# Performance work log

Measured on AMD Instinct MI355X. Metric: run time of the kernel, lower is better.

Reference implementation:

```python
import jax, jax.numpy as jnp
import numpy as np

SIGMA = 4.0
KSIZE = 2 * int(4.0 * SIGMA + 0.5) + 1  # 33, anomalib AnomalyMapGenerator default


def _gauss_kernel():
    x = jnp.arange(KSIZE, dtype=jnp.float32) - (KSIZE - 1) / 2.0
    g = jnp.exp(-0.5 * (x / SIGMA) ** 2)
    return g / g.sum()


def _blur(img):
    # img: (B,1,H,W); separable Gaussian with reflect padding (kornia border_type='reflect')
    k = _gauss_kernel()
    p = (KSIZE - 1) // 2
    dn = ('NCHW', 'OIHW', 'NCHW')
    x = jnp.pad(img, ((0, 0), (0, 0), (p, p), (0, 0)), mode='reflect')
    x = jax.lax.conv_general_dilated(x, k.reshape(1, 1, KSIZE, 1), (1, 1), 'VALID', dimension_numbers=dn)
    x = jnp.pad(x, ((0, 0), (0, 0), (0, 0), (p, p)), mode='reflect')
    return jax.lax.conv_general_dilated(x, k.reshape(1, 1, 1, KSIZE), (1, 1), 'VALID', dimension_numbers=dn)


def _edist(x, y):
    # ||x-y||_2 via expanded quadratic, clamped at 0 (matches torch euclidean_dist)
    x2 = jnp.sum(x * x, axis=-1, keepdims=True)
    y2 = jnp.sum(y * y, axis=-1, keepdims=True)
    d2 = x2 - 2.0 * (x @ y.T) + y2.T
    return jnp.sqrt(jnp.clip(d2, 0.0))


def setup_inputs() -> dict:
    key = jax.random.key(0)
    k1, k2 = jax.random.split(key)
    return {
        'embedding': jax.random.normal(k1, (6272, 128), dtype=jnp.float32),
        'memory_bank': jax.random.normal(k2, (32768, 128), dtype=jnp.float32),
        'batch_size': 8,
        'width': 28,
        'height': 28,
        'out_size': 224,
        'num_neighbors': 9,
    }


def reference(embedding, memory_bank, batch_size, width, height, out_size, num_neighbors):
    N, D = embedding.shape
    M = memory_bank.shape[0]
    # --- nearest_neighbors(embedding, n_neighbors=1), euclidean metric ---
    dist = _edist(embedding, memory_bank)            # (N, M) dominant intermediate
    patch_scores = jnp.min(dist, axis=1)             # (N,)
    locations = jnp.argmin(dist, axis=1)             # (N,)
    P = N // batch_size
    patch_scores = patch_scores.reshape(batch_size, P)
    locations = locations.reshape(batch_size, P)
    # --- compute_anomaly_score (num_neighbors > 1 branch) ---
    b_idx = jnp.arange(batch_size)
    max_p = jnp.argmax(patch_scores, axis=1)                         # (B,)
    max_feat = embedding.reshape(batch_size, P, D)[b_idx, max_p]     # (B, D)
    score = patch_scores[b_idx, max_p]                               # (B,)
    nn_idx = locations[b_idx, max_p]                                 # (B,)
    nn_sample = memory_bank[nn_idx]                                  # (B, D)
    k = min(int(num_neighbors), M)
    d_nn = _edist(nn_sample, memory_bank)                            # (B, M)
    _, support = jax.lax.top_k(-d_nn, k)                             # (B, k) smallest distances
    mem_s = memory_bank[support]                                     # (B, k, D)
    qm = jnp.einsum('bd,bkd->bk', max_feat, mem_s)
    d2 = jnp.sum(max_feat * max_feat, -1, keepdims=True) - 2.0 * qm + jnp.sum(mem_s * mem_s, -1)
    dists = jnp.sqrt(jnp.clip(d2, 0.0))                              # (B, k)
    weights = (1.0 - jax.nn.softmax(dists, axis=1))[:, 0]
    pred_score = weights * score                                     # (B,)
    # --- anomaly map: bilinear upsample (align_corners=False) + Gaussian blur ---
    pm = patch_scores.reshape(batch_size, 1, width, height)
    amap = jax.image.resize(pm, (batch_size, 1, out_size, out_size), method='bilinear')
    anomaly_map = _blur(amap)
    return pred_score, anomaly_map
```

## Files before the change

### kernel.cpp

```cpp
#include <hip/hip_runtime.h>
#include <hip/hip_bf16.h>

#define N_EMB   6272
#define M_BANK  32768
#define D_DIM   128
#define KPA     128
#define KPB     128
#define BATCH   8
#define P_PATCH 784
#define GRID_WH 28
#define OUT_WH  224
#define KNN     9
#define KSIZE   33
#define KRAD    16

typedef unsigned long long ull;
typedef short bf16x8 __attribute__((ext_vector_type(8)));
typedef float f32x4  __attribute__((ext_vector_type(4)));

#define WS_MINPACK 0
#define WS_X2      50176
#define WS_Y2      75264
#define WS_BSCORE  231424
#define WS_BMAXP   231456
#define WS_BNN     231488
#define WS_DNN     231552
#define WS_APK     2885888
#define WS_BPK     7702784
#define WS_CAND    32868608

__device__ __forceinline__ ull umin64(ull a, ull b) { return a < b ? a : b; }
__device__ __forceinline__ ull umax64(ull a, ull b) { return a > b ? a : b; }

__device__ __forceinline__ void gload_lds16(const void* g, void* l) {
    __builtin_amdgcn_global_load_lds(
        (const __attribute__((address_space(1))) void*)g,
        (__attribute__((address_space(3))) void*)l, 16, 0, 0);
}

__device__ unsigned tpf_ctr = 0;

__global__ __launch_bounds__(256) void prep_kernel(
    const float* __restrict__ emb, const float* __restrict__ bank,
    unsigned short* __restrict__ Apk, unsigned short* __restrict__ Bpk,
    float* __restrict__ x2, float* __restrict__ y2, ull* __restrict__ minpack)
{
    const int tid = threadIdx.x;
    int gi = blockIdx.x * 256 + tid;
    if (gi < N_EMB) minpack[gi] = ~0ull;

    const int w    = blockIdx.x * 4 + (tid >> 6);
    const int lane = tid & 63;

    const float* src;
    unsigned short* dst;
    float* sq;
    if (w < N_EMB) {
        src = emb + (size_t)w * D_DIM;
        dst = Apk + (size_t)w * KPA;
        sq  = x2 + w;
    } else {
        int m = w - N_EMB;
        src = bank + (size_t)m * D_DIM;
        dst = Bpk + (size_t)m * KPB;
        sq  = y2 + m;
    }
    float2 v = *(const float2*)&src[2 * lane];
    __hip_bfloat16 h0 = __float2bfloat16(v.x);
    __hip_bfloat16 h1 = __float2bfloat16(v.y);
    unsigned hb0 = *(unsigned short*)&h0, hb1 = *(unsigned short*)&h1;
    *(unsigned*)&dst[2 * lane] = hb0 | (hb1 << 16);

    float s = fmaf(v.x, v.x, v.y * v.y);
    #pragma unroll
    for (int off = 32; off > 0; off >>= 1) s += __shfl_down(s, off, 64);
    if (lane == 0) *sq = s;
}

__global__ __launch_bounds__(256, 4) void mfma_min_kernel(
    const unsigned short* __restrict__ Apk, const unsigned short* __restrict__ Bpk,
    const float* __restrict__ y2, ull* __restrict__ minpack)
{
    __shared__ __align__(16) unsigned short smem[4 * 128 * 32];
    const int PAN = 128 * 32;

    const int tid  = threadIdx.x;
    const int lane = tid & 63;
    const int wave = tid >> 6;
    const int wr = wave >> 1, wc = wave & 1;
    const int n0 = blockIdx.y * 128;
    const int m0 = blockIdx.x * 128;

    const int srow = tid >> 2;
    const int sseg = tid & 3;
    const int ssw  = sseg ^ ((srow >> 1) & 3);

    const int qa = lane >> 4;
    const int ra = lane & 15;
    const int qsw = qa ^ ((ra >> 1) & 3);

    f32x4 acc[4][4];
    #pragma unroll
    for (int i = 0; i < 4; ++i)
        #pragma unroll
        for (int j = 0; j < 4; ++j)
            acc[i][j] = (f32x4){0.f, 0.f, 0.f, 0.f};

    const unsigned short* gA = Apk + (size_t)(n0 + srow) * KPA + ssw * 8;
    const unsigned short* gB = Bpk + (size_t)(m0 + srow) * KPB + ssw * 8;
    const int lof0 = srow * 32 + sseg * 8;
    const int lof1 = (srow + 64) * 32 + sseg * 8;

    gload_lds16(gA,            &smem[lof0]);
    gload_lds16(gA + 64 * KPA, &smem[lof1]);
    gload_lds16(gB,            &smem[2 * PAN + lof0]);
    gload_lds16(gB + 64 * KPB, &smem[2 * PAN + lof1]);

    #define STEP(s, VM) { \
         \
         \
        asm volatile("s_waitcnt lgkmcnt(0)" ::: "memory"); \
        __builtin_amdgcn_sched_barrier(0); \
         \
        asm volatile("s_barrier" ::: "memory"); \
        if ((s) < 3) { \
            const int ko = ((s) + 1) * 32; \
            const int nb = ((s) + 1) & 1; \
            gload_lds16(gA + ko,            &smem[nb * PAN + lof0]); \
            gload_lds16(gA + ko + 64 * KPA, &smem[nb * PAN + lof1]); \
            gload_lds16(gB + ko,            &smem[(2 + nb) * PAN + lof0]); \
            gload_lds16(gB + ko + 64 * KPB, &smem[(2 + nb) * PAN + lof1]); \
        } \
         \
        asm volatile("s_waitcnt vmcnt(" #VM ")" ::: "memory"); \
         \
        asm volatile("s_barrier" ::: "memory"); \
        const unsigned short* As = &smem[((s) & 1) * PAN]; \
        const unsigned short* Bs = &smem[(2 + ((s) & 1)) * PAN]; \
        bf16x8 bfr[4]; \
        _Pragma("unroll") \
        for (int j = 0; j < 4; ++j) \
            bfr[j] = *(const bf16x8*)&Bs[(wc * 64 + j * 16 + ra) * 32 + qsw * 8]; \
        { \
            bf16x8 af0 = *(const bf16x8*)&As[(wr * 64 +  0 + ra) * 32 + qsw * 8]; \
            bf16x8 af1 = *(const bf16x8*)&As[(wr * 64 + 16 + ra) * 32 + qsw * 8]; \
            _Pragma("unroll") \
            for (int j = 0; j < 4; ++j) \
                acc[0][j] = __builtin_amdgcn_mfma_f32_16x16x32_bf16(af0, bfr[j], acc[0][j], 0, 0, 0); \
            _Pragma("unroll") \
            for (int j = 0; j < 4; ++j) \
                acc[1][j] = __builtin_amdgcn_mfma_f32_16x16x32_bf16(af1, bfr[j], acc[1][j], 0, 0, 0); \
            __builtin_amdgcn_sched_barrier(0); \
            bf16x8 af2 = *(const bf16x8*)&As[(wr * 64 + 32 + ra) * 32 + qsw * 8]; \
            bf16x8 af3 = *(const bf16x8*)&As[(wr * 64 + 48 + ra) * 32 + qsw * 8]; \
            _Pragma("unroll") \
            for (int j = 0; j < 4; ++j) \
                acc[2][j] = __builtin_amdgcn_mfma_f32_16x16x32_bf16(af2, bfr[j], acc[2][j], 0, 0, 0); \
            _Pragma("unroll") \
            for (int j = 0; j < 4; ++j) \
                acc[3][j] = __builtin_amdgcn_mfma_f32_16x16x32_bf16(af3, bfr[j], acc[3][j], 0, 0, 0); \
        } \
    }

    STEP(0, 4) STEP(1, 4) STEP(2, 4) STEP(3, 0)
    #undef STEP

    float y2k[4];
    unsigned mj[4];
    #pragma unroll
    for (int j = 0; j < 4; ++j) {
        const int m = m0 + wc * 64 + j * 16 + ra;
        y2k[j] = y2[m] + 1000.0f;
        mj[j]  = (unsigned)m;
    }

    ull (*red2)[32] = (ull (*)[32])smem;

    __syncthreads();

    #pragma unroll
    for (int i = 0; i < 4; ++i) {
        #pragma unroll
        for (int r = 0; r < 4; ++r) {
            const int rowl = wr * 64 + i * 16 + qa * 4 + r;
            ull mn = ~0ull;
            #pragma unroll
            for (int j = 0; j < 4; ++j) {
                float key = fmaf(-2.0f, acc[i][j][r], y2k[j]);
                ull p = ((ull)__float_as_uint(key) << 32) | mj[j];
                mn = umin64(mn, p);
            }
            red2[rowl][wc * 16 + ra] = mn;
        }
    }
    __syncthreads();
    if (tid < 128) {
        const int l = tid & 63;
        ull mn = ~0ull;
        #pragma unroll
        for (int k = 0; k < 32; ++k)
            mn = umin64(mn, red2[tid][(k + l) & 31]);
        atomicMin(&minpack[n0 + tid], mn);
    }
}

__device__ __forceinline__ int refl224(int i) {
    if (i < 0) i = -i;
    if (i >= OUT_WH) i = 2 * (OUT_WH - 1) - i;
    return i;
}

__global__ __launch_bounds__(256) void blur_argmax_kernel(
    const ull* __restrict__ minpack, const float* __restrict__ x2,
    float* __restrict__ bscore, int* __restrict__ bmaxp, int* __restrict__ bnn,
    float* __restrict__ outp)
{
    __shared__ float g[KSIZE];
    __shared__ float ps[P_PATCH];
    __shared__ float q[GRID_WH * OUT_WH];
    __shared__ float hq[GRID_WH * OUT_WH];
    __shared__ float wrow[32][GRID_WH];
    __shared__ ull red[256];

    const int tid = threadIdx.x;
    const int band = blockIdx.x;
    const int b    = blockIdx.y;

    if (tid < KSIZE) {
        float x = (tid - KRAD) * 0.25f;
        g[tid] = __expf(-0.5f * x * x);
    }
    ull local = 0;
    for (int i = tid; i < P_PATCH; i += 256) {
        ull mp = minpack[b * P_PATCH + i];
        float key = __uint_as_float((unsigned)(mp >> 32));
        float d2 = key - 1000.0f + x2[b * P_PATCH + i];
        float sc = sqrtf(fmaxf(d2, 0.0f));
        ps[i] = sc;
        ull pk = ((ull)__float_as_uint(sc) << 32) | (unsigned)(i ^ 0xFFFFFFFFu);
        local = umax64(local, pk);
    }
    red[tid] = local;
    __syncthreads();
    if (tid == 0) {
        float s = 0.0f;
        for (int i = 0; i < KSIZE; ++i) s += g[i];
        float inv = 1.0f / s;
        for (int i = 0; i < KSIZE; ++i) g[i] *= inv;
    }
    for (int s = 128; s > 0; s >>= 1) {
        if (tid < s) red[tid] = umax64(red[tid], red[tid + s]);
        __syncthreads();
    }
    if (band == 0 && tid == 0) {
        ull r = red[0];
        int p = (int)(((unsigned)(r & 0xFFFFFFFFu)) ^ 0xFFFFFFFFu);
        bscore[b] = __uint_as_float((unsigned)(r >> 32));
        bmaxp[b]  = p;
        bnn[b]    = (int)(minpack[b * P_PATCH + p] & 0xFFFFFFFFu);
    }

    for (int i = tid; i < GRID_WH * OUT_WH; i += 256) {
        int gy = i / OUT_WH, x = i - gy * OUT_WH;
        float cx = (2 * x - 7) * 0.0625f;
        int ix = (int)floorf(cx); float fx = cx - ix;
        int x0 = min(max(ix, 0), GRID_WH - 1), x1 = min(max(ix + 1, 0), GRID_WH - 1);
        q[i] = ps[gy * GRID_WH + x0] * (1.0f - fx) + ps[gy * GRID_WH + x1] * fx;
    }

    if (tid < 32) {
        int y = band * 32 + tid;
        for (int gy = 0; gy < GRID_WH; ++gy) wrow[tid][gy] = 0.0f;
        for (int t = 0; t < KSIZE; ++t) {
            int yy = refl224(y - KRAD + t);
            float cy = (2 * yy - 7) * 0.0625f;
            int iy = (int)floorf(cy); float fy = cy - iy;
            int y0 = min(max(iy, 0), GRID_WH - 1), y1 = min(max(iy + 1, 0), GRID_WH - 1);
            wrow[tid][y0] += g[t] * (1.0f - fy);
            wrow[tid][y1] += g[t] * fy;
        }
    }
    __syncthreads();

    for (int i = tid; i < GRID_WH * OUT_WH; i += 256) {
        int gy = i / OUT_WH, x = i - gy * OUT_WH;
        float s = 0.0f;
        #pragma unroll
        for (int t = 0; t < KSIZE; ++t)
            s = fmaf(g[t], q[gy * OUT_WH + refl224(x - KRAD + t)], s);
        hq[i] = s;
    }
    __syncthreads();

    const int yl = tid >> 3;
    const int xbase = (tid & 7) * 28;
    const int y = band * 32 + yl;
    float* orow = outp + ((size_t)b * OUT_WH + y) * OUT_WH;
    for (int i = 0; i < 28; ++i) {
        int x = xbase + i;
        float s = 0.0f;
        #pragma unroll
        for (int gy = 0; gy < GRID_WH; ++gy)
            s = fmaf(wrow[yl][gy], hq[gy * OUT_WH + x], s);
        orow[x] = s;
    }
}

__global__ __launch_bounds__(256) void dnn_kernel(
    const float* __restrict__ bank, const float* __restrict__ y2,
    const int* __restrict__ bnn, float* __restrict__ dnn)
{
    __shared__ float nn[BATCH][D_DIM];
    __shared__ float nny2[BATCH];
    int tid = threadIdx.x;
    for (int i = tid; i < BATCH * D_DIM; i += 256) {
        int b = i >> 7, d = i & 127;
        nn[b][d] = bank[(size_t)bnn[b] * D_DIM + d];
    }
    if (tid < BATCH) nny2[tid] = y2[bnn[tid]];
    __syncthreads();

    int w = tid >> 6, lane = tid & 63;
    int m = blockIdx.x * 4 + w;
    float2 v = *(const float2*)&bank[(size_t)m * D_DIM + 2 * lane];
    float part[BATCH];
    #pragma unroll
    for (int b = 0; b < BATCH; ++b)
        part[b] = fmaf(v.x, nn[b][2 * lane], v.y * nn[b][2 * lane + 1]);
    #pragma unroll
    for (int b = 0; b < BATCH; ++b) {
        float s = part[b];
        #pragma unroll
        for (int off = 32; off > 0; off >>= 1) s += __shfl_down(s, off, 64);
        if (lane == 0) {
            float d2 = nny2[b] + y2[m] - 2.0f * s;
            dnn[b * M_BANK + m] = sqrtf(fmaxf(d2, 0.0f));
        }
    }
}

__global__ __launch_bounds__(256) void topk_part_kernel(
    const float* __restrict__ dnn, ull* __restrict__ cand,
    const float* __restrict__ emb, const float* __restrict__ bank,
    const float* __restrict__ x2, const float* __restrict__ y2,
    const float* __restrict__ bscore, const int* __restrict__ bmaxp,
    float* __restrict__ out)
{
    __shared__ ull vals[1024];
    __shared__ ull red[256];
    __shared__ unsigned lastflag;
    const int tid = threadIdx.x;
    const int b = blockIdx.y, ch = blockIdx.x;
    const int base = ch * 1024;

    #pragma unroll
    for (int j = 0; j < 4; ++j) {
        int i = base + tid + j * 256;
        vals[tid + j * 256] = ((ull)__float_as_uint(dnn[b * M_BANK + i]) << 32) | (unsigned)i;
    }
    __syncthreads();

    for (int k = 0; k < KNN; ++k) {
        ull local = vals[tid];
        #pragma unroll
        for (int j = 1; j < 4; ++j) local = umin64(local, vals[tid + j * 256]);
        red[tid] = local;
        __syncthreads();
        for (int s = 128; s > 0; s >>= 1) {
            if (tid < s) red[tid] = umin64(red[tid], red[tid + s]);
            __syncthreads();
        }
        ull win = red[0];
        if (tid == 0) cand[(b * 32 + ch) * KNN + k] = win;
        #pragma unroll
        for (int j = 0; j < 4; ++j)
            if (vals[tid + j * 256] == win) vals[tid + j * 256] = ~0ull;
        __syncthreads();
    }

    if (tid == 0) {
        __threadfence();
        unsigned t = atomicAdd(&tpf_ctr, 1u);
        lastflag = (t == 8u * 32u - 1u);
    }
    __syncthreads();
    if (!lastflag) return;
    __threadfence();

    const int wv = tid >> 6, ln = tid & 63;
    #pragma unroll
    for (int half = 0; half < 2; ++half) {
        const int bb = wv + half * 4;
        const ull* cb = cand + (size_t)bb * 32 * KNN;
        ull c0 = cb[ln];
        ull c1 = cb[ln + 64];
        ull c2 = cb[ln + 128];
        ull c3 = cb[ln + 192];
        ull c4 = (ln < 32) ? cb[ln + 256] : ~0ull;
        const int e = bb * P_PATCH + bmaxp[bb];
        const float mf0 = emb[(size_t)e * D_DIM + 2 * ln];
        const float mf1 = emb[(size_t)e * D_DIM + 2 * ln + 1];
        const float xe = x2[e];
        float dists[KNN];
        #pragma unroll
        for (int k = 0; k < KNN; ++k) {
            ull mn = umin64(umin64(umin64(c0, c1), umin64(c2, c3)), c4);
            #pragma unroll
            for (int s = 1; s < 64; s <<= 1)
                mn = umin64(mn, (ull)__shfl_xor((unsigned long long)mn, s, 64));
            if (c0 == mn) c0 = ~0ull;
            if (c1 == mn) c1 = ~0ull;
            if (c2 == mn) c2 = ~0ull;
            if (c3 == mn) c3 = ~0ull;
            if (c4 == mn) c4 = ~0ull;
            const int m = (int)(mn & 0xFFFFFFFFu);
            float dot = fmaf(mf0, bank[(size_t)m * D_DIM + 2 * ln],
                             mf1 * bank[(size_t)m * D_DIM + 2 * ln + 1]);
            #pragma unroll
            for (int s = 1; s < 64; s <<= 1)
                dot += __shfl_xor(dot, s, 64);
            float d2 = xe - 2.0f * dot + y2[m];
            dists[k] = sqrtf(fmaxf(d2, 0.0f));
        }
        if (ln == 0) {
            float mx = dists[0];
            #pragma unroll
            for (int k = 1; k < KNN; ++k) mx = fmaxf(mx, dists[k]);
            float ssum = 0.0f;
            #pragma unroll
            for (int k = 0; k < KNN; ++k) ssum += expf(dists[k] - mx);
            float wgt = 1.0f - expf(dists[0] - mx) / ssum;
            out[bb] = wgt * bscore[bb];
        }
    }
    if (tid == 0) atomicExch(&tpf_ctr, 0u);
}

extern "C" void kernel_launch(void* const* d_in, const int* in_sizes, int n_in,
                              void* d_out, int out_size, void* d_ws, size_t ws_size,
                              hipStream_t stream) {
    const float* emb  = (const float*)d_in[0];
    const float* bank = (const float*)d_in[1];
    float* out = (float*)d_out;

    char* ws = (char*)d_ws;
    ull*   minpack = (ull*)(ws + WS_MINPACK);
    float* x2      = (float*)(ws + WS_X2);
    float* y2      = (float*)(ws + WS_Y2);
    float* bscore  = (float*)(ws + WS_BSCORE);
    int*   bmaxp   = (int*)(ws + WS_BMAXP);
    int*   bnn     = (int*)(ws + WS_BNN);
    float* dnn     = (float*)(ws + WS_DNN);
    unsigned short* Apk = (unsigned short*)(ws + WS_APK);
    unsigned short* Bpk = (unsigned short*)(ws + WS_BPK);
    ull*   cand    = (ull*)(ws + WS_CAND);

    prep_kernel<<<(N_EMB + M_BANK) / 4, 256, 0, stream>>>(emb, bank, Apk, Bpk, x2, y2, minpack);
    {
        dim3 grid(M_BANK / 128, N_EMB / 128);
        mfma_min_kernel<<<grid, 256, 0, stream>>>(Apk, Bpk, y2, minpack);
    }
    {
        dim3 grid(OUT_WH / 32, BATCH);
        blur_argmax_kernel<<<grid, 256, 0, stream>>>(minpack, x2, bscore, bmaxp, bnn, out + BATCH);
    }
    dnn_kernel<<<M_BANK / 4, 256, 0, stream>>>(bank, y2, bnn, dnn);
    {
        dim3 grid(32, BATCH);
        topk_part_kernel<<<grid, 256, 0, stream>>>(dnn, cand, emb, bank, x2, y2, bscore, bmaxp, out);
    }
}
```

Before: 232.9 us.

## Fold per-batch argmax into GEMM tail and merge blur with top-k

The per-batch argmax of patch scores moves into the last-finishing block of the MFMA min kernel, found with an atomic counter, so dnn_kernel no longer waits on the blur kernel. Blur and partial top-k then run together in one launch with a shared-memory union, which cuts one kernel launch and lets the blur overlap the top-k work. The cost is an extra atomic and fence in every GEMM block, plus a serial tail run by a single block.

```diff
diff --git a/kernel.cpp b/kernel.cpp
--- a/kernel.cpp
+++ b/kernel.cpp
@@ -13,6 +13,7 @@
 #define KNN     9
 #define KSIZE   33
 #define KRAD    16
+#define MFM_BLOCKS (256 * 49)
 
 typedef unsigned long long ull;
 typedef short bf16x8 __attribute__((ext_vector_type(8)));
@@ -39,6 +40,7 @@
 }
 
 __device__ unsigned tpf_ctr = 0;
+__device__ unsigned mfm_ctr = 0;
 
 __global__ __launch_bounds__(256) void prep_kernel(
     const float* __restrict__ emb, const float* __restrict__ bank,
@@ -79,9 +81,12 @@
 
 __global__ __launch_bounds__(256, 4) void mfma_min_kernel(
     const unsigned short* __restrict__ Apk, const unsigned short* __restrict__ Bpk,
-    const float* __restrict__ y2, ull* __restrict__ minpack)
+    const float* __restrict__ y2, const float* __restrict__ x2,
+    ull* __restrict__ minpack,
+    float* __restrict__ bscore, int* __restrict__ bmaxp, int* __restrict__ bnn)
 {
     __shared__ __align__(16) unsigned short smem[4 * 128 * 32];
+    __shared__ unsigned amflag;
     const int PAN = 128 * 32;
 
     const int tid  = threadIdx.x;
@@ -202,6 +207,75 @@
             mn = umin64(mn, red2[tid][(k + l) & 31]);
         atomicMin(&minpack[n0 + tid], mn);
     }
+
+    if (tid == 0) {
+        __threadfence();
+        unsigned t = atomicAdd(&mfm_ctr, 1u);
+        amflag = (t == (unsigned)MFM_BLOCKS - 1u);
+    }
+    __syncthreads();
+    if (!amflag) return;
+    __threadfence();
+
+    {
+        const int wv2 = tid >> 6, ln2 = tid & 63;
+        #pragma unroll
+        for (int half = 0; half < 2; ++half) {
+            const int bb = wv2 + half * 4;
+            ull best = 0;
+            for (int i = ln2; i < P_PATCH; i += 64) {
+                ull mp = minpack[bb * P_PATCH + i];
+                float key = __uint_as_float((unsigned)(mp >> 32));
+                float d2 = key - 1000.0f + x2[bb * P_PATCH + i];
+                float sc = sqrtf(fmaxf(d2, 0.0f));
+                ull pk = ((ull)__float_as_uint(sc) << 32) | (unsigned)(i ^ 0xFFFFFFFFu);
+                best = umax64(best, pk);
+            }
+            #pragma unroll
+            for (int s = 1; s < 64; s <<= 1)
+                best = umax64(best, (ull)__shfl_xor((unsigned long long)best, s, 64));
+            if (ln2 == 0) {
+                int p = (int)(((unsigned)(best & 0xFFFFFFFFu)) ^ 0xFFFFFFFFu);
+                bscore[bb] = __uint_as_float((unsigned)(best >> 32));
+                bmaxp[bb]  = p;
+                bnn[bb]    = (int)(minpack[bb * P_PATCH + p] & 0xFFFFFFFFu);
+            }
+        }
+    }
+    if (tid == 0) atomicExch(&mfm_ctr, 0u);
+}
+
+__global__ __launch_bounds__(256) void dnn_kernel(
+    const float* __restrict__ bank, const float* __restrict__ y2,
+    const int* __restrict__ bnn, float* __restrict__ dnn)
+{
+    __shared__ float nn[BATCH][D_DIM];
+    __shared__ float nny2[BATCH];
+    int tid = threadIdx.x;
+    for (int i = tid; i < BATCH * D_DIM; i += 256) {
+        int b = i >> 7, d = i & 127;
+        nn[b][d] = bank[(size_t)bnn[b] * D_DIM + d];
+    }
+    if (tid < BATCH) nny2[tid] = y2[bnn[tid]];
+    __syncthreads();
+
+    int w = tid >> 6, lane = tid & 63;
+    int m = blockIdx.x * 4 + w;
+    float2 v = *(const float2*)&bank[(size_t)m * D_DIM + 2 * lane];
+    float part[BATCH];
+    #pragma unroll
+    for (int b = 0; b < BATCH; ++b)
+        part[b] = fmaf(v.x, nn[b][2 * lane], v.y * nn[b][2 * lane + 1]);
+    #pragma unroll
+    for (int b = 0; b < BATCH; ++b) {
+        float s = part[b];
+        #pragma unroll
+        for (int off = 32; off > 0; off >>= 1) s += __shfl_down(s, off, 64);
+        if (lane == 0) {
+            float d2 = nny2[b] + y2[m] - 2.0f * s;
+            dnn[b * M_BANK + m] = sqrtf(fmaxf(d2, 0.0f));
+        }
+    }
 }
 
 __device__ __forceinline__ int refl224(int i) {
@@ -210,37 +284,141 @@
     return i;
 }
 
-__global__ __launch_bounds__(256) void blur_argmax_kernel(
+union SharedU {
+    struct {
+        float g[KSIZE];
+        float ps[P_PATCH];
+        float q[GRID_WH * OUT_WH];
+        float hq[GRID_WH * OUT_WH];
+        float wrow[32][GRID_WH];
+    } blur;
+    struct {
+        ull vals[1024];
+        ull red[256];
+    } topk;
+};
+
+__global__ __launch_bounds__(256) void blur_topk_kernel(
     const ull* __restrict__ minpack, const float* __restrict__ x2,
-    float* __restrict__ bscore, int* __restrict__ bmaxp, int* __restrict__ bnn,
-    float* __restrict__ outp)
+    const float* __restrict__ dnn, ull* __restrict__ cand,
+    const float* __restrict__ emb, const float* __restrict__ bank,
+    const float* __restrict__ y2,
+    const float* __restrict__ bscore, const int* __restrict__ bmaxp,
+    float* __restrict__ out)
 {
-    __shared__ float g[KSIZE];
-    __shared__ float ps[P_PATCH];
-    __shared__ float q[GRID_WH * OUT_WH];
-    __shared__ float hq[GRID_WH * OUT_WH];
-    __shared__ float wrow[32][GRID_WH];
-    __shared__ ull red[256];
-
+    __shared__ SharedU su;
+    __shared__ unsigned lastflag;
     const int tid = threadIdx.x;
-    const int band = blockIdx.x;
-    const int b    = blockIdx.y;
+    const int b = blockIdx.y;
+
+    if (blockIdx.x < 32) {
+        const int ch = blockIdx.x;
+        const int base = ch * 1024;
+        ull* vals = su.topk.vals;
+        ull* red  = su.topk.red;
+
+        #pragma unroll
+        for (int j = 0; j < 4; ++j) {
+            int i = base + tid + j * 256;
+            vals[tid + j * 256] = ((ull)__float_as_uint(dnn[b * M_BANK + i]) << 32) | (unsigned)i;
+        }
+        __syncthreads();
+
+        for (int k = 0; k < KNN; ++k) {
+            ull local = vals[tid];
+            #pragma unroll
+            for (int j = 1; j < 4; ++j) local = umin64(local, vals[tid + j * 256]);
+            red[tid] = local;
+            __syncthreads();
+            for (int s = 128; s > 0; s >>= 1) {
+                if (tid < s) red[tid] = umin64(red[tid], red[tid + s]);
+                __syncthreads();
+            }
+            ull win = red[0];
+            if (tid == 0) cand[(b * 32 + ch) * KNN + k] = win;
+            #pragma unroll
+            for (int j = 0; j < 4; ++j)
+                if (vals[tid + j * 256] == win) vals[tid + j * 256] = ~0ull;
+            __syncthreads();
+        }
+
+        if (tid == 0) {
+            __threadfence();
+            unsigned t = atomicAdd(&tpf_ctr, 1u);
+            lastflag = (t == 8u * 32u - 1u);
+        }
+        __syncthreads();
+        if (!lastflag) return;
+        __threadfence();
+
+        const int wv = tid >> 6, ln = tid & 63;
+        #pragma unroll
+        for (int half = 0; half < 2; ++half) {
+            const int bb = wv + half * 4;
+            const ull* cb = cand + (size_t)bb * 32 * KNN;
+            ull c0 = cb[ln];
+            ull c1 = cb[ln + 64];
+            ull c2 = cb[ln + 128];
+            ull c3 = cb[ln + 192];
+            ull c4 = (ln < 32) ? cb[ln + 256] : ~0ull;
+            const int e = bb * P_PATCH + bmaxp[bb];
+            const float mf0 = emb[(size_t)e * D_DIM + 2 * ln];
+            const float mf1 = emb[(size_t)e * D_DIM + 2 * ln + 1];
+            const float xe = x2[e];
+            float dists[KNN];
+            #pragma unroll
+            for (int k = 0; k < KNN; ++k) {
+                ull mn = umin64(umin64(umin64(c0, c1), umin64(c2, c3)), c4);
+                #pragma unroll
+                for (int s = 1; s < 64; s <<= 1)
+                    mn = umin64(mn, (ull)__shfl_xor((unsigned long long)mn, s, 64));
+                if (c0 == mn) c0 = ~0ull;
+                if (c1 == mn) c1 = ~0ull;
+                if (c2 == mn) c2 = ~0ull;
+                if (c3 == mn) c3 = ~0ull;
+                if (c4 == mn) c4 = ~0ull;
+                const int m = (int)(mn & 0xFFFFFFFFu);
+                float dot = fmaf(mf0, bank[(size_t)m * D_DIM + 2 * ln],
+                                 mf1 * bank[(size_t)m * D_DIM + 2 * ln + 1]);
+                #pragma unroll
+                for (int s = 1; s < 64; s <<= 1)
+                    dot += __shfl_xor(dot, s, 64);
+                float d2 = xe - 2.0f * dot + y2[m];
+                dists[k] = sqrtf(fmaxf(d2, 0.0f));
+            }
+            if (ln == 0) {
+                float mx = dists[0];
+                #pragma unroll
+                for (int k = 1; k < KNN; ++k) mx = fmaxf(mx, dists[k]);
+                float ssum = 0.0f;
+                #pragma unroll
+                for (int k = 0; k < KNN; ++k) ssum += expf(dists[k] - mx);
+                float wgt = 1.0f - expf(dists[0] - mx) / ssum;
+                out[bb] = wgt * bscore[bb];
+            }
+        }
+        if (tid == 0) atomicExch(&tpf_ctr, 0u);
+        return;
+    }
+
+    const int band = blockIdx.x - 32;
+    float* g    = su.blur.g;
+    float* ps   = su.blur.ps;
+    float* q    = su.blur.q;
+    float* hq   = su.blur.hq;
+    float (*wrow)[GRID_WH] = su.blur.wrow;
+    float* outp = out + BATCH;
 
     if (tid < KSIZE) {
         float x = (tid - KRAD) * 0.25f;
         g[tid] = __expf(-0.5f * x * x);
     }
-    ull local = 0;
     for (int i = tid; i < P_PATCH; i += 256) {
         ull mp = minpack[b * P_PATCH + i];
         float key = __uint_as_float((unsigned)(mp >> 32));
         float d2 = key - 1000.0f + x2[b * P_PATCH + i];
-        float sc = sqrtf(fmaxf(d2, 0.0f));
-        ps[i] = sc;
-        ull pk = ((ull)__float_as_uint(sc) << 32) | (unsigned)(i ^ 0xFFFFFFFFu);
-        local = umax64(local, pk);
-    }
-    red[tid] = local;
+        ps[i] = sqrtf(fmaxf(d2, 0.0f));
+    }
     __syncthreads();
     if (tid == 0) {
         float s = 0.0f;
@@ -248,17 +426,7 @@
         float inv = 1.0f / s;
         for (int i = 0; i < KSIZE; ++i) g[i] *= inv;
     }
-    for (int s = 128; s > 0; s >>= 1) {
-        if (tid < s) red[tid] = umax64(red[tid], red[tid + s]);
-        __syncthreads();
-    }
-    if (band == 0 && tid == 0) {
-        ull r = red[0];
-        int p = (int)(((unsigned)(r & 0xFFFFFFFFu)) ^ 0xFFFFFFFFu);
-        bscore[b] = __uint_as_float((unsigned)(r >> 32));
-        bmaxp[b]  = p;
-        bnn[b]    = (int)(minpack[b * P_PATCH + p] & 0xFFFFFFFFu);
-    }
+    __syncthreads();
 
     for (int i = tid; i < GRID_WH * OUT_WH; i += 256) {
         int gy = i / OUT_WH, x = i - gy * OUT_WH;
@@ -304,136 +472,6 @@
             s = fmaf(wrow[yl][gy], hq[gy * OUT_WH + x], s);
         orow[x] = s;
     }
-}
-
-__global__ __launch_bounds__(256) void dnn_kernel(
-    const float* __restrict__ bank, const float* __restrict__ y2,
-    const int* __restrict__ bnn, float* __restrict__ dnn)
-{
-    __shared__ float nn[BATCH][D_DIM];
-    __shared__ float nny2[BATCH];
-    int tid = threadIdx.x;
-    for (int i = tid; i < BATCH * D_DIM; i += 256) {
-        int b = i >> 7, d = i & 127;
-        nn[b][d] = bank[(size_t)bnn[b] * D_DIM + d];
-    }
-    if (tid < BATCH) nny2[tid] = y2[bnn[tid]];
-    __syncthreads();
-
-    int w = tid >> 6, lane = tid & 63;
-    int m = blockIdx.x * 4 + w;
-    float2 v = *(const float2*)&bank[(size_t)m * D_DIM + 2 * lane];
-    float part[BATCH];
-    #pragma unroll
-    for (int b = 0; b < BATCH; ++b)
-        part[b] = fmaf(v.x, nn[b][2 * lane], v.y * nn[b][2 * lane + 1]);
-    #pragma unroll
-    for (int b = 0; b < BATCH; ++b) {
-        float s = part[b];
-        #pragma unroll
-        for (int off = 32; off > 0; off >>= 1) s += __shfl_down(s, off, 64);
-        if (lane == 0) {
-            float d2 = nny2[b] + y2[m] - 2.0f * s;
-            dnn[b * M_BANK + m] = sqrtf(fmaxf(d2, 0.0f));
-        }
-    }
-}
-
-__global__ __launch_bounds__(256) void topk_part_kernel(
-    const float* __restrict__ dnn, ull* __restrict__ cand,
-    const float* __restrict__ emb, const float* __restrict__ bank,
-    const float* __restrict__ x2, const float* __restrict__ y2,
-    const float* __restrict__ bscore, const int* __restrict__ bmaxp,
-    float* __restrict__ out)
-{
-    __shared__ ull vals[1024];
-    __shared__ ull red[256];
-    __shared__ unsigned lastflag;
-    const int tid = threadIdx.x;
-    const int b = blockIdx.y, ch = blockIdx.x;
-    const int base = ch * 1024;
-
-    #pragma unroll
-    for (int j = 0; j < 4; ++j) {
-        int i = base + tid + j * 256;
-        vals[tid + j * 256] = ((ull)__float_as_uint(dnn[b * M_BANK + i]) << 32) | (unsigned)i;
-    }
-    __syncthreads();
-
-    for (int k = 0; k < KNN; ++k) {
-        ull local = vals[tid];
-        #pragma unroll
-        for (int j = 1; j < 4; ++j) local = umin64(local, vals[tid + j * 256]);
-        red[tid] = local;
-        __syncthreads();
-        for (int s = 128; s > 0; s >>= 1) {
-            if (tid < s) red[tid] = umin64(red[tid], red[tid + s]);
-            __syncthreads();
-        }
-        ull win = red[0];
-        if (tid == 0) cand[(b * 32 + ch) * KNN + k] = win;
-        #pragma unroll
-        for (int j = 0; j < 4; ++j)
-            if (vals[tid + j * 256] == win) vals[tid + j * 256] = ~0ull;
-        __syncthreads();
-    }
-
-    if (tid == 0) {
-        __threadfence();
-        unsigned t = atomicAdd(&tpf_ctr, 1u);
-        lastflag = (t == 8u * 32u - 1u);
-    }
-    __syncthreads();
-    if (!lastflag) return;
-    __threadfence();
-
-    const int wv = tid >> 6, ln = tid & 63;
-    #pragma unroll
-    for (int half = 0; half < 2; ++half) {
-        const int bb = wv + half * 4;
-        const ull* cb = cand + (size_t)bb * 32 * KNN;
-        ull c0 = cb[ln];
-        ull c1 = cb[ln + 64];
-        ull c2 = cb[ln + 128];
-        ull c3 = cb[ln + 192];
-        ull c4 = (ln < 32) ? cb[ln + 256] : ~0ull;
-        const int e = bb * P_PATCH + bmaxp[bb];
-        const float mf0 = emb[(size_t)e * D_DIM + 2 * ln];
-        const float mf1 = emb[(size_t)e * D_DIM + 2 * ln + 1];
-        const float xe = x2[e];
-        float dists[KNN];
-        #pragma unroll
-        for (int k = 0; k < KNN; ++k) {
-            ull mn = umin64(umin64(umin64(c0, c1), umin64(c2, c3)), c4);
-            #pragma unroll
-            for (int s = 1; s < 64; s <<= 1)
-                mn = umin64(mn, (ull)__shfl_xor((unsigned long long)mn, s, 64));
-            if (c0 == mn) c0 = ~0ull;
-            if (c1 == mn) c1 = ~0ull;
-            if (c2 == mn) c2 = ~0ull;
-            if (c3 == mn) c3 = ~0ull;
-            if (c4 == mn) c4 = ~0ull;
-            const int m = (int)(mn & 0xFFFFFFFFu);
-            float dot = fmaf(mf0, bank[(size_t)m * D_DIM + 2 * ln],
-                             mf1 * bank[(size_t)m * D_DIM + 2 * ln + 1]);
-            #pragma unroll
-            for (int s = 1; s < 64; s <<= 1)
-                dot += __shfl_xor(dot, s, 64);
-            float d2 = xe - 2.0f * dot + y2[m];
-            dists[k] = sqrtf(fmaxf(d2, 0.0f));
-        }
-        if (ln == 0) {
-            float mx = dists[0];
-            #pragma unroll
-            for (int k = 1; k < KNN; ++k) mx = fmaxf(mx, dists[k]);
-            float ssum = 0.0f;
-            #pragma unroll
-            for (int k = 0; k < KNN; ++k) ssum += expf(dists[k] - mx);
-            float wgt = 1.0f - expf(dists[0] - mx) / ssum;
-            out[bb] = wgt * bscore[bb];
-        }
-    }
-    if (tid == 0) atomicExch(&tpf_ctr, 0u);
 }
 
 extern "C" void kernel_launch(void* const* d_in, const int* in_sizes, int n_in,
@@ -458,15 +496,11 @@
     prep_kernel<<<(N_EMB + M_BANK) / 4, 256, 0, stream>>>(emb, bank, Apk, Bpk, x2, y2, minpack);
     {
         dim3 grid(M_BANK / 128, N_EMB / 128);
-        mfma_min_kernel<<<grid, 256, 0, stream>>>(Apk, Bpk, y2, minpack);
-    }
-    {
-        dim3 grid(OUT_WH / 32, BATCH);
-        blur_argmax_kernel<<<grid, 256, 0, stream>>>(minpack, x2, bscore, bmaxp, bnn, out + BATCH);
+        mfma_min_kernel<<<grid, 256, 0, stream>>>(Apk, Bpk, y2, x2, minpack, bscore, bmaxp, bnn);
     }
     dnn_kernel<<<M_BANK / 4, 256, 0, stream>>>(bank, y2, bnn, dnn);
     {
-        dim3 grid(32, BATCH);
-        topk_part_kernel<<<grid, 256, 0, stream>>>(dnn, cand, emb, bank, x2, y2, bscore, bmaxp, out);
-    }
-}
+        dim3 grid(32 + OUT_WH / 32, BATCH);
+        blur_topk_kernel<<<grid, 256, 0, stream>>>(minpack, x2, dnn, cand, emb, bank, y2, bscore, bmaxp, out);
+    }
+}
```

After: 422.8 us. +81.6%, slower.
